# Optimization experiments

Hardware: AMD Instinct MI355X
Metric: run time of the kernel (lower is better)

The kernel has to match this reference:

```python
import jax, jax.numpy as jnp
import numpy as np

DIM = 256
H_GLOBAL = 8
H_LOCAL = 4  # max(1, num_heads // 2)
WINDOW = 5
HALF = WINDOW // 2
B, S = 4, 2048
EPS = 1e-5


def layer_norm(x, g, b):
    mu = jnp.mean(x, axis=-1, keepdims=True)
    var = jnp.mean(jnp.square(x - mu), axis=-1, keepdims=True)
    return (x - mu) * jax.lax.rsqrt(var + EPS) * g + b


def qkv_proj(x, in_w, in_b):
    qkv = x @ in_w.T + in_b
    return jnp.split(qkv, 3, axis=-1)


def global_mha(x, in_w, in_b, out_w, out_b, nh):
    Bq, Sq, D = x.shape
    hd = D // nh
    q, k, v = qkv_proj(x, in_w, in_b)
    q = q.reshape(Bq, Sq, nh, hd)
    k = k.reshape(Bq, Sq, nh, hd)
    v = v.reshape(Bq, Sq, nh, hd)
    scores = jnp.einsum('bqhd,bkhd->bhqk', q, k) / np.sqrt(hd).astype(np.float32)
    attn = jax.nn.softmax(scores, axis=-1)
    o = jnp.einsum('bhqk,bkhd->bqhd', attn, v).reshape(Bq, Sq, D)
    return o @ out_w.T + out_b


def local_mha(x, in_w, in_b, out_w, out_b, nh):
    # banded sliding-window attention, window = 2*HALF+1, per-query softmax
    Bq, Sq, D = x.shape
    hd = D // nh
    q, k, v = qkv_proj(x, in_w, in_b)
    kp = jnp.pad(k, ((0, 0), (HALF, HALF), (0, 0)))
    vp = jnp.pad(v, ((0, 0), (HALF, HALF), (0, 0)))
    # [B, S, W, D] windows of keys/values around each query position
    k_win = jnp.stack([kp[:, j:j + Sq] for j in range(WINDOW)], axis=2)
    v_win = jnp.stack([vp[:, j:j + Sq] for j in range(WINDOW)], axis=2)
    q = q.reshape(Bq, Sq, nh, hd)
    k_win = k_win.reshape(Bq, Sq, WINDOW, nh, hd)
    v_win = v_win.reshape(Bq, Sq, WINDOW, nh, hd)
    scores = jnp.einsum('bshd,bswhd->bshw', q, k_win) / np.sqrt(hd).astype(np.float32)
    idx = jnp.arange(Sq)[:, None] + jnp.arange(-HALF, HALF + 1)[None, :]  # [S, W]
    valid = (idx >= 0) & (idx < Sq)
    scores = jnp.where(valid[None, :, None, :], scores, -jnp.inf)
    attn = jax.nn.softmax(scores, axis=-1)
    o = jnp.einsum('bshw,bswhd->bshd', attn, v_win).reshape(Bq, Sq, D)
    return o @ out_w.T + out_b


def setup_inputs() -> dict:
    key = jax.random.key(0)
    ks = jax.random.split(key, 8)
    sc = 0.02
    d = DIM
    return {
        'x': jax.random.normal(ks[0], (B, S, d), jnp.float32),
        'g_in_w': jax.random.normal(ks[1], (3 * d, d), jnp.float32) * sc,
        'g_in_b': jnp.zeros((3 * d,), jnp.float32),
        'g_out_w': jax.random.normal(ks[2], (d, d), jnp.float32) * sc,
        'g_out_b': jnp.zeros((d,), jnp.float32),
        't_in_w': jax.random.normal(ks[3], (3 * d, d), jnp.float32) * sc,
        't_in_b': jnp.zeros((3 * d,), jnp.float32),
        't_out_w': jax.random.normal(ks[4], (d, d), jnp.float32) * sc,
        't_out_b': jnp.zeros((d,), jnp.float32),
        'fus_w1': jax.random.normal(ks[5], (2 * d, 2 * d), jnp.float32) * sc,
        'fus_b1': jnp.zeros((2 * d,), jnp.float32),
        'fus_w2': jax.random.normal(ks[6], (d, 2 * d), jnp.float32) * sc,
        'fus_b2': jnp.zeros((d,), jnp.float32),
        'ffn_w1': jax.random.normal(ks[7], (2 * d, d), jnp.float32) * sc,
        'ffn_b1': jnp.zeros((2 * d,), jnp.float32),
        'ffn_w2': jax.random.normal(jax.random.fold_in(key, 9), (d, 2 * d), jnp.float32) * sc,
        'ffn_b2': jnp.zeros((d,), jnp.float32),
        'gn_g': jnp.ones((d,), jnp.float32),
        'gn_b': jnp.zeros((d,), jnp.float32),
        'fn_g': jnp.ones((d,), jnp.float32),
        'fn_b': jnp.zeros((d,), jnp.float32),
    }


def reference(x, g_in_w, g_in_b, g_out_w, g_out_b,
              t_in_w, t_in_b, t_out_w, t_out_b,
              fus_w1, fus_b1, fus_w2, fus_b2,
              ffn_w1, ffn_b1, ffn_w2, ffn_b2,
              gn_g, gn_b, fn_g, fn_b):
    x_global = global_mha(x, g_in_w, g_in_b, g_out_w, g_out_b, H_GLOBAL)
    x_local = local_mha(x, t_in_w, t_in_b, t_out_w, t_out_b, H_LOCAL)
    x_comb = jnp.concatenate([x_global, x_local], axis=-1)
    x_fused = jax.nn.silu(x_comb @ fus_w1.T + fus_b1) @ fus_w2.T + fus_b2
    x = layer_norm(x + x_fused, gn_g, gn_b)
    x_ffn = jax.nn.silu(x @ ffn_w1.T + ffn_b1) @ ffn_w2.T + ffn_b2
    x = layer_norm(x + x_ffn, fn_g, fn_b)
    return x
```

## Files before the change

kernel.cpp:

```cpp
#include <hip/hip_runtime.h>

constexpr int Bb = 4;
constexpr int Ss = 2048;
constexpr int QSTR = 1536;

typedef __bf16 bf16x8 __attribute__((ext_vector_type(8)));
typedef __bf16 bf16x4 __attribute__((ext_vector_type(4)));
typedef float  f32x4  __attribute__((ext_vector_type(4)));
typedef unsigned int uint2v __attribute__((ext_vector_type(2)));
typedef unsigned int uint4v __attribute__((ext_vector_type(4)));

__device__ __forceinline__ void glds16(const void* g, void* l) {
    __builtin_amdgcn_global_load_lds(
        (const __attribute__((address_space(1))) unsigned int*)g,
        (__attribute__((address_space(3))) unsigned int*)l, 16, 0, 0);
}

__device__ __forceinline__ void xpose4(unsigned int& a, unsigned int& b) {
    uint2v r = __builtin_amdgcn_permlane32_swap(a, b, false, false);
    uint2v u = __builtin_amdgcn_permlane16_swap(r[0], r[1], false, false);
    a = u[0]; b = u[1];
}

__device__ __forceinline__ unsigned int exp2_pk(float a, float b) {
    float ea = __builtin_amdgcn_exp2f(a);
    float eb = __builtin_amdgcn_exp2f(b);
    unsigned int r;
    asm("v_cvt_pk_bf16_f32 %0, %1, %2" : "=v"(r) : "v"(ea), "v"(eb));
    return r;
}

struct CvtArgs {
    const float* src[9];
    __bf16* dst[9];
    int start[10];
};

__global__ __launch_bounds__(256) void convert_all(CvtArgs a)
{
    int e = 0;
    const int bid = blockIdx.x;
#pragma unroll
    for (int i = 0; i < 8; i++) if (bid >= a.start[i + 1]) e = i + 1;
    const int idx = (bid - a.start[e]) * 256 + threadIdx.x;
    const float* s = a.src[e];
    float4 v0 = *(const float4*)&s[(size_t)idx * 8];
    float4 v1 = *(const float4*)&s[(size_t)idx * 8 + 4];
    bf16x8 o;
    o[0] = (__bf16)v0.x; o[1] = (__bf16)v0.y; o[2] = (__bf16)v0.z; o[3] = (__bf16)v0.w;
    o[4] = (__bf16)v1.x; o[5] = (__bf16)v1.y; o[6] = (__bf16)v1.z; o[7] = (__bf16)v1.w;
    *(bf16x8*)&a.dst[e][(size_t)idx * 8] = o;
}

__global__ __launch_bounds__(256) void gemm128(
    const __bf16* __restrict__ A, const __bf16* __restrict__ W,
    const float* __restrict__ bias, const float* __restrict__ bias2, int bsplit,
    __bf16* __restrict__ C, int K, int ldc)
{
    __shared__ __bf16 As[128 * 64];
    __shared__ __bf16 Ws[128 * 64];
    const int tid = threadIdx.x;
    const int lane = tid & 63;
    const int wv = tid >> 6;
    const int wm = (wv >> 1) * 64;
    const int wn = (wv & 1) * 64;
    const int qrow = lane & 15;
    const int quad = lane >> 4;
    const int n0 = blockIdx.x * 128;
    const int m0 = blockIdx.y * 128;

    f32x4 acc[4][4];
#pragma unroll
    for (int i = 0; i < 4; i++)
#pragma unroll
        for (int j = 0; j < 4; j++) acc[i][j] = {0.f, 0.f, 0.f, 0.f};

    for (int k0 = 0; k0 < K; k0 += 64) {
        __syncthreads();
#pragma unroll
        for (int i = 0; i < 4; i++) {
            const int c = (wv * 4 + i) * 64 + lane;
            const int row = c >> 3, g = c & 7;
            const int gs = (g ^ (row & 7)) * 8;
            glds16(&A[(size_t)(m0 + row) * K + k0 + gs], &As[(wv * 4 + i) * 512]);
            glds16(&W[(size_t)(n0 + row) * K + k0 + gs], &Ws[(wv * 4 + i) * 512]);
        }
        __syncthreads();
#pragma unroll
        for (int ksub = 0; ksub < 2; ksub++) {
            const int gl = ksub * 4 + quad;
            bf16x8 af[4], bf[4];
#pragma unroll
            for (int mi = 0; mi < 4; mi++) {
                const int row = wm + mi * 16 + qrow;
                af[mi] = *(const bf16x8*)&As[row * 64 + (gl ^ (row & 7)) * 8];
            }
#pragma unroll
            for (int ni = 0; ni < 4; ni++) {
                const int row = wn + ni * 16 + qrow;
                bf[ni] = *(const bf16x8*)&Ws[row * 64 + (gl ^ (row & 7)) * 8];
            }
#pragma unroll
            for (int mi = 0; mi < 4; mi++)
#pragma unroll
                for (int ni = 0; ni < 4; ni++)
                    acc[mi][ni] = __builtin_amdgcn_mfma_f32_16x16x32_bf16(
                        af[mi], bf[ni], acc[mi][ni], 0, 0, 0);
        }
    }

    float bz[4];
#pragma unroll
    for (int ni = 0; ni < 4; ni++) {
        const int n = n0 + wn + ni * 16 + qrow;
        bz[ni] = (n < bsplit) ? bias[n] : bias2[n - bsplit];
    }
#pragma unroll
    for (int mi = 0; mi < 4; mi++)
#pragma unroll
        for (int r = 0; r < 4; r++) {
            const int row = m0 + wm + mi * 16 + quad * 4 + r;
#pragma unroll
            for (int ni = 0; ni < 4; ni++) {
                float v = acc[mi][ni][r] + bz[ni];
                C[(size_t)row * ldc + n0 + wn + ni * 16 + qrow] = (__bf16)v;
            }
        }
}

template<bool SILU, bool OUT_BF16>
__global__ __launch_bounds__(256) void gemm_mid(
    const __bf16* __restrict__ A0, const __bf16* __restrict__ W0,
    const float* __restrict__ bias0, const __bf16* __restrict__ W1,
    const float* __restrict__ bias1, int nsplit, int aoff1, int coff1,
    void* __restrict__ C, int lda, int K, int ldc)
{
    __shared__ __bf16 As[64 * 128];
    __shared__ __bf16 Ws[64 * 128];
    const int tid = threadIdx.x;
    const int lane = tid & 63;
    const int wv = tid >> 6;
    const int wm = (wv >> 1) * 32;
    const int wn = (wv & 1) * 32;
    const int qrow = lane & 15;
    const int quad = lane >> 4;
    const bool second = (int)blockIdx.x >= nsplit;
    const int bx = second ? (blockIdx.x - nsplit) : blockIdx.x;
    const __bf16* A = second ? (A0 + aoff1) : A0;
    const __bf16* W = second ? W1 : W0;
    const float* bias = second ? bias1 : bias0;
    const int coff = second ? coff1 : 0;
    const int n0 = bx * 64;
    const int m0 = blockIdx.y * 64;

    f32x4 acc[2][2];
#pragma unroll
    for (int i = 0; i < 2; i++)
#pragma unroll
        for (int j = 0; j < 2; j++) acc[i][j] = {0.f, 0.f, 0.f, 0.f};

    for (int k0 = 0; k0 < K; k0 += 128) {
        __syncthreads();
#pragma unroll
        for (int i = 0; i < 4; i++) {
            const int c = (wv * 4 + i) * 64 + lane;
            const int row = c >> 4, s = c & 15;
            const int gs = ((s & 8) | ((s ^ row) & 7)) * 8;
            glds16(&A[(size_t)(m0 + row) * lda + k0 + gs], &As[(wv * 4 + i) * 512]);
            glds16(&W[(size_t)(n0 + row) * K + k0 + gs], &Ws[(wv * 4 + i) * 512]);
        }
        __syncthreads();
#pragma unroll
        for (int ksub = 0; ksub < 4; ksub++) {
            const int gl = ksub * 4 + quad;
            bf16x8 af[2], bf[2];
#pragma unroll
            for (int mi = 0; mi < 2; mi++) {
                const int row = wm + mi * 16 + qrow;
                const int s = (gl & 8) | ((gl ^ row) & 7);
                af[mi] = *(const bf16x8*)&As[row * 128 + s * 8];
            }
#pragma unroll
            for (int ni = 0; ni < 2; ni++) {
                const int row = wn + ni * 16 + qrow;
                const int s = (gl & 8) | ((gl ^ row) & 7);
                bf[ni] = *(const bf16x8*)&Ws[row * 128 + s * 8];
            }
#pragma unroll
            for (int mi = 0; mi < 2; mi++)
#pragma unroll
                for (int ni = 0; ni < 2; ni++)
                    acc[mi][ni] = __builtin_amdgcn_mfma_f32_16x16x32_bf16(
                        af[mi], bf[ni], acc[mi][ni], 0, 0, 0);
        }
    }

    float bz[2];
#pragma unroll
    for (int ni = 0; ni < 2; ni++) bz[ni] = bias[n0 + wn + ni * 16 + qrow];

#pragma unroll
    for (int mi = 0; mi < 2; mi++)
#pragma unroll
        for (int r = 0; r < 4; r++) {
            const int row = m0 + wm + mi * 16 + quad * 4 + r;
#pragma unroll
            for (int ni = 0; ni < 2; ni++) {
                float v = acc[mi][ni][r] + bz[ni];
                if (SILU) v = v / (1.f + __expf(-v));
                const int col = coff + n0 + wn + ni * 16 + qrow;
                if (OUT_BF16)
                    ((__bf16*)C)[(size_t)row * ldc + col] = (__bf16)v;
                else
                    ((float*)C)[(size_t)row * ldc + col] = v;
            }
        }
}

__global__ __launch_bounds__(512) void attn_fused(
    const __bf16* __restrict__ qkv, __bf16* __restrict__ Op,
    float* __restrict__ Lp, __bf16* __restrict__ acat)
{
    __shared__ __bf16 Kl[2][64 * 32];
    __shared__ __bf16 Vt[2][32 * 72];

    const int t = threadIdx.x;
    const int lane = t & 63;
    const int wv = t >> 6;

    if (blockIdx.x < 1024) {
        const int bid = blockIdx.x;
        const int sp = bid & 3;
        const int qc = (bid >> 2) & 7;
        const int h  = (bid >> 5) & 7;
        const int b  = bid >> 8;
        const int bS = b * Ss;
        const int q0 = qc * 256;

        const int qrow = lane & 15;
        const int quad = lane >> 4;
        const float cQ = 1.4426950408889634f * 0.17677669529663687f;

        bf16x8 qf[2];
#pragma unroll
        for (int tl = 0; tl < 2; tl++) {
            bf16x8 qraw = *(const bf16x8*)(qkv +
                (size_t)(bS + q0 + wv * 32 + tl * 16 + qrow) * QSTR + h * 32 + quad * 8);
#pragma unroll
            for (int i = 0; i < 8; i++) qf[tl][i] = (__bf16)((float)qraw[i] * cQ);
        }
        bf16x8 ones;
#pragma unroll
        for (int i = 0; i < 8; i++) ones[i] = (__bf16)1.0f;

        f32x4 o0[2], o1[2], lac[2];
#pragma unroll
        for (int tl = 0; tl < 2; tl++) {
            o0[tl] = {0.f, 0.f, 0.f, 0.f};
            o1[tl] = {0.f, 0.f, 0.f, 0.f};
            lac[tl] = {0.f, 0.f, 0.f, 0.f};
        }
        const f32x4 z = {0.f, 0.f, 0.f, 0.f};

        const int kc_c = wv * 64 + lane;
        const int kkey = kc_c >> 2, kdg = kc_c & 3;
        const int vkey = t & 63, vq = t >> 6;
        const int kc0 = sp * 8;

        bf16x4 vreg = *(const bf16x4*)(qkv +
            (size_t)(bS + kc0 * 64 + vkey) * QSTR + 512 + h * 32 + vq * 4);
        if (wv < 4)
            glds16(qkv + (size_t)(bS + kc0 * 64 + kkey) * QSTR + 256 + h * 32 + kdg * 8,
                   &Kl[0][wv * 512]);

        for (int i = 0; i < 8; i++) {
            const int cur = i & 1;
#pragma unroll
            for (int e = 0; e < 4; e++) Vt[cur][(vq * 4 + e) * 72 + vkey] = vreg[e];
            __syncthreads();
            const int nx = (i < 7) ? (kc0 + i + 1) : (kc0 + 7);
            vreg = *(const bf16x4*)(qkv +
                (size_t)(bS + nx * 64 + vkey) * QSTR + 512 + h * 32 + vq * 4);
            if (i < 7 && wv < 4)
                glds16(qkv + (size_t)(bS + nx * 64 + kkey) * QSTR + 256 + h * 32 + kdg * 8,
                       &Kl[1 - cur][wv * 512]);

            bf16x8 kf[4];
#pragma unroll
            for (int kg = 0; kg < 4; kg++)
                kf[kg] = *(const bf16x8*)&Kl[cur][(kg * 16 + qrow) * 32 + quad * 8];
            bf16x8 vf00 = *(const bf16x8*)&Vt[cur][qrow * 72 + quad * 8];
            bf16x8 vf01 = *(const bf16x8*)&Vt[cur][qrow * 72 + 32 + quad * 8];
            bf16x8 vf10 = *(const bf16x8*)&Vt[cur][(16 + qrow) * 72 + quad * 8];
            bf16x8 vf11 = *(const bf16x8*)&Vt[cur][(16 + qrow) * 72 + 32 + quad * 8];

#pragma unroll
            for (int tl = 0; tl < 2; tl++) {
                f32x4 s[4];
#pragma unroll
                for (int kg = 0; kg < 4; kg++)
                    s[kg] = __builtin_amdgcn_mfma_f32_16x16x32_bf16(
                        kf[kg], qf[tl], z, 0, 0, 0);
                unsigned int R[4][2];
#pragma unroll
                for (int kg = 0; kg < 4; kg++) {
                    R[kg][0] = exp2_pk(s[kg][0], s[kg][1]);
                    R[kg][1] = exp2_pk(s[kg][2], s[kg][3]);
                }
                xpose4(R[0][0], R[1][0]);
                xpose4(R[0][1], R[1][1]);
                xpose4(R[2][0], R[3][0]);
                xpose4(R[2][1], R[3][1]);
                uint4v p0u = {R[0][0], R[0][1], R[1][0], R[1][1]};
                uint4v p1u = {R[2][0], R[2][1], R[3][0], R[3][1]};
                bf16x8 pf0 = __builtin_bit_cast(bf16x8, p0u);
                bf16x8 pf1 = __builtin_bit_cast(bf16x8, p1u);

                o0[tl] = __builtin_amdgcn_mfma_f32_16x16x32_bf16(vf00, pf0, o0[tl], 0, 0, 0);
                o1[tl] = __builtin_amdgcn_mfma_f32_16x16x32_bf16(vf10, pf0, o1[tl], 0, 0, 0);
                lac[tl] = __builtin_amdgcn_mfma_f32_16x16x32_bf16(ones, pf0, lac[tl], 0, 0, 0);
                o0[tl] = __builtin_amdgcn_mfma_f32_16x16x32_bf16(vf01, pf1, o0[tl], 0, 0, 0);
                o1[tl] = __builtin_amdgcn_mfma_f32_16x16x32_bf16(vf11, pf1, o1[tl], 0, 0, 0);
                lac[tl] = __builtin_amdgcn_mfma_f32_16x16x32_bf16(ones, pf1, lac[tl], 0, 0, 0);
            }
        }

#pragma unroll
        for (int tl = 0; tl < 2; tl++) {
            const int gid = (b * 8 + h) * 2048 + q0 + wv * 32 + tl * 16 + qrow;
            __bf16* po = Op + (size_t)sp * 2097152 + (size_t)gid * 32;
            bf16x4 w0, w1;
#pragma unroll
            for (int r = 0; r < 4; r++) {
                w0[r] = (__bf16)o0[tl][r];
                w1[r] = (__bf16)o1[tl][r];
            }
            *(bf16x4*)&po[quad * 4]      = w0;
            *(bf16x4*)&po[16 + quad * 4] = w1;
            if (quad == 0) Lp[sp * 65536 + gid] = lac[tl][0];
        }
    } else {
        const int w = (blockIdx.x - 1024) * 8 + wv;
        const int g = lane >> 3;
        const int l8 = lane & 7;
        const int R = w * 8 + g;
        const int h = R & 3;
        const int s = (R >> 2) & 2047;
        const int b = R >> 13;

        float qv[8];
        {
            bf16x8 q8 = *(const bf16x8*)&qkv[(size_t)(b * Ss + s) * QSTR + 768 + h * 64 + l8 * 8];
#pragma unroll
            for (int e = 0; e < 8; e++) qv[e] = (float)q8[e];
        }

        float sc[5];
        bf16x8 v8[5];
#pragma unroll
        for (int j = 0; j < 5; j++) {
            int pos = s + j - 2;
            bool valid = (pos >= 0) && (pos < Ss);
            int cpos = valid ? pos : 0;
            const size_t rb = (size_t)(b * Ss + cpos) * QSTR;
            bf16x8 k8 = *(const bf16x8*)&qkv[rb + 1024 + h * 64 + l8 * 8];
            v8[j]     = *(const bf16x8*)&qkv[rb + 1280 + h * 64 + l8 * 8];
            float p = 0.f;
#pragma unroll
            for (int e = 0; e < 8; e++) p += qv[e] * (float)k8[e];
            p += __shfl_xor(p, 1, 64);
            p += __shfl_xor(p, 2, 64);
            p += __shfl_xor(p, 4, 64);
            sc[j] = valid ? p * 0.125f : -1e30f;
        }
        float m = sc[0];
#pragma unroll
        for (int j = 1; j < 5; j++) m = fmaxf(m, sc[j]);
        float l = 0.f;
        float o[8];
#pragma unroll
        for (int e = 0; e < 8; e++) o[e] = 0.f;
#pragma unroll
        for (int j = 0; j < 5; j++) {
            float pe = __builtin_amdgcn_exp2f((sc[j] - m) * 1.4426950408889634f);
            l += pe;
#pragma unroll
            for (int e = 0; e < 8; e++) o[e] += pe * (float)v8[j][e];
        }
        const float li = 1.f / l;
        bf16x8 r;
#pragma unroll
        for (int e = 0; e < 8; e++) r[e] = (__bf16)(o[e] * li);
        *(bf16x8*)&acat[(size_t)(b * Ss + s) * 512 + 256 + h * 64 + l8 * 8] = r;
    }
}

__global__ __launch_bounds__(256) void attn_combine(
    const __bf16* __restrict__ Op, const float* __restrict__ Lp,
    __bf16* __restrict__ acat)
{
    const int t = blockIdx.x * 256 + threadIdx.x;
    const int gid = t >> 3;
    const int dg = t & 7;
    const int b = gid >> 14;
    const int h = (gid >> 11) & 7;
    const int q = gid & 2047;

    const float li = 1.f / (Lp[gid] + Lp[65536 + gid] +
                            Lp[131072 + gid] + Lp[196608 + gid]);
    const __bf16* base = Op + (size_t)gid * 32 + dg * 4;
    bf16x4 a0 = *(const bf16x4*)&base[0];
    bf16x4 a1 = *(const bf16x4*)&base[2097152];
    bf16x4 a2 = *(const bf16x4*)&base[4194304];
    bf16x4 a3 = *(const bf16x4*)&base[6291456];
    bf16x4 r;
#pragma unroll
    for (int i = 0; i < 4; i++)
        r[i] = (__bf16)(((float)a0[i] + (float)a1[i] +
                         (float)a2[i] + (float)a3[i]) * li);
    *(bf16x4*)&acat[(size_t)(b * Ss + q) * 512 + h * 32 + dg * 4] = r;
}

__global__ __launch_bounds__(256) void ln_residual(
    const float* __restrict__ a, const __bf16* __restrict__ r,
    const float* __restrict__ g, const float* __restrict__ be,
    float* __restrict__ out, __bf16* __restrict__ ob)
{
    const int lane = threadIdx.x & 63;
    const int tok = blockIdx.x * 4 + (threadIdx.x >> 6);
    float4 xa = ((const float4*)a)[(size_t)tok * 64 + lane];
    bf16x4 xr = *(const bf16x4*)&r[(size_t)tok * 256 + lane * 4];
    float4 x;
    x.x = xa.x + (float)xr[0]; x.y = xa.y + (float)xr[1];
    x.z = xa.z + (float)xr[2]; x.w = xa.w + (float)xr[3];
    float sum = x.x + x.y + x.z + x.w;
#pragma unroll
    for (int off = 32; off > 0; off >>= 1) sum += __shfl_xor(sum, off, 64);
    float mu = sum * (1.f / 256.f);
    float4 c;
    c.x = x.x - mu; c.y = x.y - mu; c.z = x.z - mu; c.w = x.w - mu;
    float sq = c.x * c.x + c.y * c.y + c.z * c.z + c.w * c.w;
#pragma unroll
    for (int off = 32; off > 0; off >>= 1) sq += __shfl_xor(sq, off, 64);
    float rs = rsqrtf(sq * (1.f / 256.f) + 1e-5f);
    float4 gg = ((const float4*)g)[lane];
    float4 bb = ((const float4*)be)[lane];
    float4 o;
    o.x = c.x * rs * gg.x + bb.x; o.y = c.y * rs * gg.y + bb.y;
    o.z = c.z * rs * gg.z + bb.z; o.w = c.w * rs * gg.w + bb.w;
    ((float4*)out)[(size_t)tok * 64 + lane] = o;
    if (ob) {
        bf16x4 hh;
        hh[0] = (__bf16)o.x; hh[1] = (__bf16)o.y; hh[2] = (__bf16)o.z; hh[3] = (__bf16)o.w;
        *(bf16x4*)&ob[(size_t)tok * 256 + lane * 4] = hh;
    }
}

extern "C" void kernel_launch(void* const* d_in, const int* in_sizes, int n_in,
                              void* d_out, int out_size, void* d_ws, size_t ws_size,
                              hipStream_t stream)
{
    const float* x      = (const float*)d_in[0];
    const float* g_in_w = (const float*)d_in[1];
    const float* g_in_b = (const float*)d_in[2];
    const float* g_out_w= (const float*)d_in[3];
    const float* g_out_b= (const float*)d_in[4];
    const float* t_in_w = (const float*)d_in[5];
    const float* t_in_b = (const float*)d_in[6];
    const float* t_out_w= (const float*)d_in[7];
    const float* t_out_b= (const float*)d_in[8];
    const float* fus_w1 = (const float*)d_in[9];
    const float* fus_b1 = (const float*)d_in[10];
    const float* fus_w2 = (const float*)d_in[11];
    const float* fus_b2 = (const float*)d_in[12];
    const float* ffn_w1 = (const float*)d_in[13];
    const float* ffn_b1 = (const float*)d_in[14];
    const float* ffn_w2 = (const float*)d_in[15];
    const float* ffn_b2 = (const float*)d_in[16];
    const float* gn_g   = (const float*)d_in[17];
    const float* gn_b   = (const float*)d_in[18];
    const float* fn_g   = (const float*)d_in[19];
    const float* fn_b   = (const float*)d_in[20];
    float* out = (float*)d_out;
    float* ws  = (float*)d_ws;

    __bf16* xb     = (__bf16*)(ws);
    __bf16* wb     = (__bf16*)(ws + 1048576);
    __bf16* qkvgl  = (__bf16*)(ws + 1638400);
    __bf16* acat   = (__bf16*)(ws + 7929856);
    __bf16* fcomb  = (__bf16*)(ws + 10027008);
    __bf16* h1     = (__bf16*)(ws + 12124160);
    __bf16* xfb    = (__bf16*)(ws + 14221312);
    float*  x2     = ws + 16318464;
    __bf16* x2b    = (__bf16*)(ws + 18415616);
    __bf16* h2     = h1;
    __bf16* xffb   = xfb;
    __bf16* Op = (__bf16*)(ws + 10027008);
    float*  Lp = ws + 18415616;

    __bf16* w_gin  = wb;
    __bf16* w_gout = wb + 393216;
    __bf16* w_tout = wb + 458752;
    __bf16* w_f1   = wb + 524288;
    __bf16* w_f2   = wb + 786432;
    __bf16* w_n1   = wb + 917504;
    __bf16* w_n2   = wb + 1048576;

    CvtArgs ca;
    ca.src[0] = x;      ca.dst[0] = xb;
    ca.src[1] = g_in_w; ca.dst[1] = w_gin;
    ca.src[2] = t_in_w; ca.dst[2] = w_gin + 196608;
    ca.src[3] = g_out_w;ca.dst[3] = w_gout;
    ca.src[4] = t_out_w;ca.dst[4] = w_tout;
    ca.src[5] = fus_w1; ca.dst[5] = w_f1;
    ca.src[6] = fus_w2; ca.dst[6] = w_f2;
    ca.src[7] = ffn_w1; ca.dst[7] = w_n1;
    ca.src[8] = ffn_w2; ca.dst[8] = w_n2;
    int st[10] = {0, 1024, 1120, 1216, 1248, 1280, 1408, 1472, 1536, 1600};
    for (int i = 0; i < 10; i++) ca.start[i] = st[i];

    convert_all<<<dim3(1600), 256, 0, stream>>>(ca);

    gemm128<<<dim3(12, 64), 256, 0, stream>>>(
        xb, w_gin, g_in_b, t_in_b, 768, qkvgl, 256, QSTR);
    attn_fused<<<dim3(1536), 512, 0, stream>>>(qkvgl, Op, Lp, acat);
    attn_combine<<<dim3(2048), 256, 0, stream>>>(Op, Lp, acat);
    gemm_mid<false, true><<<dim3(8, 128), 256, 0, stream>>>(
        acat, w_gout, g_out_b, w_tout, t_out_b, 4, 256, 256, fcomb, 512, 256, 512);
    gemm_mid<true,  true><<<dim3(8, 128), 256, 0, stream>>>(
        fcomb, w_f1, fus_b1, w_f1, fus_b1, 1 << 30, 0, 0, h1, 512, 512, 512);
    gemm_mid<false, true><<<dim3(4, 128), 256, 0, stream>>>(
        h1, w_f2, fus_b2, w_f2, fus_b2, 1 << 30, 0, 0, xfb, 512, 512, 256);
    ln_residual<<<dim3(2048), 256, 0, stream>>>(x, xfb, gn_g, gn_b, x2, x2b);
    gemm_mid<true,  true><<<dim3(8, 128), 256, 0, stream>>>(
        x2b, w_n1, ffn_b1, w_n1, ffn_b1, 1 << 30, 0, 0, h2, 256, 256, 512);
    gemm_mid<false, true><<<dim3(4, 128), 256, 0, stream>>>(
        h2, w_n2, ffn_b2, w_n2, ffn_b2, 1 << 30, 0, 0, xffb, 512, 512, 256);
    ln_residual<<<dim3(2048), 256, 0, stream>>>(x2, xffb, fn_g, fn_b, out, nullptr);
}
```

Measured before the change: 210.7 us.

## Fuse attention combine, projections, MLPs and layernorms into one per-token epilogue kernel

Replaces the attention-combine kernel, six mid-size GEMM launches and two layernorm kernels with a single epilogue kernel. Each 64-thread wavefront handles 16 tokens and keeps all intermediate activations in registers, chaining MFMA stages through a transpose-pack helper. Weights are read straight from global memory without LDS staging. This removes many launches and the intermediate HBM round-trips, but it brings heavy register pressure, only 512 single-wave blocks (low occupancy), and repeated uncoalesced weight reads from cache.

```diff
diff --git a/kernel.cpp b/kernel.cpp
--- a/kernel.cpp
+++ b/kernel.cpp
@@ -22,12 +22,88 @@
     a = u[0]; b = u[1];
 }
 
+__device__ __forceinline__ unsigned int cvtpk(float a, float b) {
+    unsigned int r;
+    asm("v_cvt_pk_bf16_f32 %0, %1, %2" : "=v"(r) : "v"(a), "v"(b));
+    return r;
+}
+
 __device__ __forceinline__ unsigned int exp2_pk(float a, float b) {
     float ea = __builtin_amdgcn_exp2f(a);
     float eb = __builtin_amdgcn_exp2f(b);
-    unsigned int r;
-    asm("v_cvt_pk_bf16_f32 %0, %1, %2" : "=v"(r) : "v"(ea), "v"(eb));
-    return r;
+    return cvtpk(ea, eb);
+}
+
+__device__ __forceinline__ bf16x8 pack_pair(f32x4 dA, f32x4 dB) {
+    unsigned int RA0 = cvtpk(dA[0], dA[1]);
+    unsigned int RA1 = cvtpk(dA[2], dA[3]);
+    unsigned int RB0 = cvtpk(dB[0], dB[1]);
+    unsigned int RB1 = cvtpk(dB[2], dB[3]);
+    xpose4(RA0, RB0);
+    xpose4(RA1, RB1);
+    uint4v u = {RA0, RA1, RB0, RB1};
+    return __builtin_bit_cast(bf16x8, u);
+}
+
+template<int NK>
+__device__ __forceinline__ void mm4(
+    const __bf16* __restrict__ W, const int K, const int ft0,
+    const bf16x8* act, const int qrow, const int quad, f32x4 acc[4])
+{
+#pragma unroll
+    for (int i = 0; i < 4; i++) acc[i] = {0.f, 0.f, 0.f, 0.f};
+#pragma unroll
+    for (int kc = 0; kc < NK; kc++) {
+        bf16x8 wf[4];
+#pragma unroll
+        for (int i = 0; i < 4; i++)
+            wf[i] = *(const bf16x8*)&W[(size_t)((ft0 + i) * 16 + qrow) * K + kc * 32 + quad * 8];
+#pragma unroll
+        for (int i = 0; i < 4; i++)
+            acc[i] = __builtin_amdgcn_mfma_f32_16x16x32_bf16(wf[i], act[kc], acc[i], 0, 0, 0);
+    }
+}
+
+template<int NK, bool SILU>
+__device__ __forceinline__ void stage_pack4(
+    const __bf16* __restrict__ W, const int K, const int ft0,
+    const float* __restrict__ bias,
+    const bf16x8* act, const int qrow, const int quad, bf16x8* outc)
+{
+    f32x4 acc[4];
+    mm4<NK>(W, K, ft0, act, qrow, quad, acc);
+#pragma unroll
+    for (int i = 0; i < 4; i++) {
+        float4 bz = *(const float4*)&bias[(ft0 + i) * 16 + quad * 4];
+        acc[i][0] += bz.x; acc[i][1] += bz.y; acc[i][2] += bz.z; acc[i][3] += bz.w;
+        if (SILU) {
+#pragma unroll
+            for (int r = 0; r < 4; r++) {
+                float v = acc[i][r];
+                acc[i][r] = v / (1.f + __builtin_amdgcn_exp2f(-v * 1.4426950408889634f));
+            }
+        }
+    }
+    outc[0] = pack_pair(acc[0], acc[1]);
+    outc[1] = pack_pair(acc[2], acc[3]);
+}
+
+template<int NK>
+__device__ __forceinline__ void stage_d4(
+    const __bf16* __restrict__ W, const int K, const int ft0,
+    const float* __restrict__ bias,
+    const bf16x8* act, const int qrow, const int quad, f32x4* dout)
+{
+    f32x4 acc[4];
+    mm4<NK>(W, K, ft0, act, qrow, quad, acc);
+#pragma unroll
+    for (int i = 0; i < 4; i++) {
+        float4 bz = *(const float4*)&bias[(ft0 + i) * 16 + quad * 4];
+        dout[i][0] = acc[i][0] + bz.x;
+        dout[i][1] = acc[i][1] + bz.y;
+        dout[i][2] = acc[i][2] + bz.z;
+        dout[i][3] = acc[i][3] + bz.w;
+    }
 }
 
 struct CvtArgs {
@@ -124,95 +200,6 @@
             for (int ni = 0; ni < 4; ni++) {
                 float v = acc[mi][ni][r] + bz[ni];
                 C[(size_t)row * ldc + n0 + wn + ni * 16 + qrow] = (__bf16)v;
-            }
-        }
-}
-
-template<bool SILU, bool OUT_BF16>
-__global__ __launch_bounds__(256) void gemm_mid(
-    const __bf16* __restrict__ A0, const __bf16* __restrict__ W0,
-    const float* __restrict__ bias0, const __bf16* __restrict__ W1,
-    const float* __restrict__ bias1, int nsplit, int aoff1, int coff1,
-    void* __restrict__ C, int lda, int K, int ldc)
-{
-    __shared__ __bf16 As[64 * 128];
-    __shared__ __bf16 Ws[64 * 128];
-    const int tid = threadIdx.x;
-    const int lane = tid & 63;
-    const int wv = tid >> 6;
-    const int wm = (wv >> 1) * 32;
-    const int wn = (wv & 1) * 32;
-    const int qrow = lane & 15;
-    const int quad = lane >> 4;
-    const bool second = (int)blockIdx.x >= nsplit;
-    const int bx = second ? (blockIdx.x - nsplit) : blockIdx.x;
-    const __bf16* A = second ? (A0 + aoff1) : A0;
-    const __bf16* W = second ? W1 : W0;
-    const float* bias = second ? bias1 : bias0;
-    const int coff = second ? coff1 : 0;
-    const int n0 = bx * 64;
-    const int m0 = blockIdx.y * 64;
-
-    f32x4 acc[2][2];
-#pragma unroll
-    for (int i = 0; i < 2; i++)
-#pragma unroll
-        for (int j = 0; j < 2; j++) acc[i][j] = {0.f, 0.f, 0.f, 0.f};
-
-    for (int k0 = 0; k0 < K; k0 += 128) {
-        __syncthreads();
-#pragma unroll
-        for (int i = 0; i < 4; i++) {
-            const int c = (wv * 4 + i) * 64 + lane;
-            const int row = c >> 4, s = c & 15;
-            const int gs = ((s & 8) | ((s ^ row) & 7)) * 8;
-            glds16(&A[(size_t)(m0 + row) * lda + k0 + gs], &As[(wv * 4 + i) * 512]);
-            glds16(&W[(size_t)(n0 + row) * K + k0 + gs], &Ws[(wv * 4 + i) * 512]);
-        }
-        __syncthreads();
-#pragma unroll
-        for (int ksub = 0; ksub < 4; ksub++) {
-            const int gl = ksub * 4 + quad;
-            bf16x8 af[2], bf[2];
-#pragma unroll
-            for (int mi = 0; mi < 2; mi++) {
-                const int row = wm + mi * 16 + qrow;
-                const int s = (gl & 8) | ((gl ^ row) & 7);
-                af[mi] = *(const bf16x8*)&As[row * 128 + s * 8];
-            }
-#pragma unroll
-            for (int ni = 0; ni < 2; ni++) {
-                const int row = wn + ni * 16 + qrow;
-                const int s = (gl & 8) | ((gl ^ row) & 7);
-                bf[ni] = *(const bf16x8*)&Ws[row * 128 + s * 8];
-            }
-#pragma unroll
-            for (int mi = 0; mi < 2; mi++)
-#pragma unroll
-                for (int ni = 0; ni < 2; ni++)
-                    acc[mi][ni] = __builtin_amdgcn_mfma_f32_16x16x32_bf16(
-                        af[mi], bf[ni], acc[mi][ni], 0, 0, 0);
-        }
-    }
-
-    float bz[2];
-#pragma unroll
-    for (int ni = 0; ni < 2; ni++) bz[ni] = bias[n0 + wn + ni * 16 + qrow];
-
-#pragma unroll
-    for (int mi = 0; mi < 2; mi++)
-#pragma unroll
-        for (int r = 0; r < 4; r++) {
-            const int row = m0 + wm + mi * 16 + quad * 4 + r;
-#pragma unroll
-            for (int ni = 0; ni < 2; ni++) {
-                float v = acc[mi][ni][r] + bz[ni];
-                if (SILU) v = v / (1.f + __expf(-v));
-                const int col = coff + n0 + wn + ni * 16 + qrow;
-                if (OUT_BF16)
-                    ((__bf16*)C)[(size_t)row * ldc + col] = (__bf16)v;
-                else
-                    ((float*)C)[(size_t)row * ldc + col] = v;
             }
         }
 }
@@ -395,64 +382,142 @@
     }
 }
 
-__global__ __launch_bounds__(256) void attn_combine(
+__global__ __launch_bounds__(64) void epilogue(
     const __bf16* __restrict__ Op, const float* __restrict__ Lp,
-    __bf16* __restrict__ acat)
-{
-    const int t = blockIdx.x * 256 + threadIdx.x;
-    const int gid = t >> 3;
-    const int dg = t & 7;
-    const int b = gid >> 14;
-    const int h = (gid >> 11) & 7;
-    const int q = gid & 2047;
-
-    const float li = 1.f / (Lp[gid] + Lp[65536 + gid] +
-                            Lp[131072 + gid] + Lp[196608 + gid]);
-    const __bf16* base = Op + (size_t)gid * 32 + dg * 4;
-    bf16x4 a0 = *(const bf16x4*)&base[0];
-    bf16x4 a1 = *(const bf16x4*)&base[2097152];
-    bf16x4 a2 = *(const bf16x4*)&base[4194304];
-    bf16x4 a3 = *(const bf16x4*)&base[6291456];
-    bf16x4 r;
-#pragma unroll
-    for (int i = 0; i < 4; i++)
-        r[i] = (__bf16)(((float)a0[i] + (float)a1[i] +
-                         (float)a2[i] + (float)a3[i]) * li);
-    *(bf16x4*)&acat[(size_t)(b * Ss + q) * 512 + h * 32 + dg * 4] = r;
-}
-
-__global__ __launch_bounds__(256) void ln_residual(
-    const float* __restrict__ a, const __bf16* __restrict__ r,
-    const float* __restrict__ g, const float* __restrict__ be,
-    float* __restrict__ out, __bf16* __restrict__ ob)
+    const __bf16* __restrict__ acat, const float* __restrict__ x,
+    const __bf16* __restrict__ w_gout, const float* __restrict__ g_out_b,
+    const __bf16* __restrict__ w_tout, const float* __restrict__ t_out_b,
+    const __bf16* __restrict__ w_f1, const float* __restrict__ fus_b1,
+    const __bf16* __restrict__ w_f2, const float* __restrict__ fus_b2,
+    const __bf16* __restrict__ w_n1, const float* __restrict__ ffn_b1,
+    const __bf16* __restrict__ w_n2, const float* __restrict__ ffn_b2,
+    const float* __restrict__ gn_g, const float* __restrict__ gn_b,
+    const float* __restrict__ fn_g, const float* __restrict__ fn_b,
+    float* __restrict__ out)
 {
     const int lane = threadIdx.x & 63;
-    const int tok = blockIdx.x * 4 + (threadIdx.x >> 6);
-    float4 xa = ((const float4*)a)[(size_t)tok * 64 + lane];
-    bf16x4 xr = *(const bf16x4*)&r[(size_t)tok * 256 + lane * 4];
-    float4 x;
-    x.x = xa.x + (float)xr[0]; x.y = xa.y + (float)xr[1];
-    x.z = xa.z + (float)xr[2]; x.w = xa.w + (float)xr[3];
-    float sum = x.x + x.y + x.z + x.w;
-#pragma unroll
-    for (int off = 32; off > 0; off >>= 1) sum += __shfl_xor(sum, off, 64);
-    float mu = sum * (1.f / 256.f);
-    float4 c;
-    c.x = x.x - mu; c.y = x.y - mu; c.z = x.z - mu; c.w = x.w - mu;
-    float sq = c.x * c.x + c.y * c.y + c.z * c.z + c.w * c.w;
-#pragma unroll
-    for (int off = 32; off > 0; off >>= 1) sq += __shfl_xor(sq, off, 64);
-    float rs = rsqrtf(sq * (1.f / 256.f) + 1e-5f);
-    float4 gg = ((const float4*)g)[lane];
-    float4 bb = ((const float4*)be)[lane];
-    float4 o;
-    o.x = c.x * rs * gg.x + bb.x; o.y = c.y * rs * gg.y + bb.y;
-    o.z = c.z * rs * gg.z + bb.z; o.w = c.w * rs * gg.w + bb.w;
-    ((float4*)out)[(size_t)tok * 64 + lane] = o;
-    if (ob) {
-        bf16x4 hh;
-        hh[0] = (__bf16)o.x; hh[1] = (__bf16)o.y; hh[2] = (__bf16)o.z; hh[3] = (__bf16)o.w;
-        *(bf16x4*)&ob[(size_t)tok * 256 + lane * 4] = hh;
+    const int qrow = lane & 15;
+    const int quad = lane >> 4;
+    const int t = blockIdx.x * 16 + qrow;
+    const int b = t >> 11;
+    const int q = t & 2047;
+
+    bf16x8 act0[16];
+#pragma unroll
+    for (int h = 0; h < 8; h++) {
+        const size_t gid = (size_t)(b * 8 + h) * 2048 + q;
+        const float li = 1.f / (Lp[gid] + Lp[65536 + gid] +
+                                Lp[131072 + gid] + Lp[196608 + gid]);
+        const __bf16* base = Op + gid * 32 + quad * 8;
+        bf16x8 a0 = *(const bf16x8*)&base[0];
+        bf16x8 a1 = *(const bf16x8*)&base[2097152];
+        bf16x8 a2 = *(const bf16x8*)&base[4194304];
+        bf16x8 a3 = *(const bf16x8*)&base[6291456];
+        unsigned int w[4];
+#pragma unroll
+        for (int p = 0; p < 4; p++) {
+            float v0 = ((float)a0[2*p]   + (float)a1[2*p]   +
+                        (float)a2[2*p]   + (float)a3[2*p])   * li;
+            float v1 = ((float)a0[2*p+1] + (float)a1[2*p+1] +
+                        (float)a2[2*p+1] + (float)a3[2*p+1]) * li;
+            w[p] = cvtpk(v0, v1);
+        }
+        uint4v u = {w[0], w[1], w[2], w[3]};
+        act0[h] = __builtin_bit_cast(bf16x8, u);
+    }
+#pragma unroll
+    for (int c = 0; c < 8; c++)
+        act0[8 + c] = *(const bf16x8*)&acat[(size_t)t * 512 + 256 + c * 32 + quad * 8];
+
+    bf16x8 act1[16];
+#pragma unroll
+    for (int g4 = 0; g4 < 4; g4++)
+        stage_pack4<8, false>(w_gout, 256, g4 * 4, g_out_b, act0, qrow, quad, &act1[g4 * 2]);
+#pragma unroll
+    for (int g4 = 0; g4 < 4; g4++)
+        stage_pack4<8, false>(w_tout, 256, g4 * 4, t_out_b, act0 + 8, qrow, quad, &act1[8 + g4 * 2]);
+
+    bf16x8 act2[16];
+#pragma unroll
+    for (int g4 = 0; g4 < 8; g4++)
+        stage_pack4<16, true>(w_f1, 512, g4 * 4, fus_b1, act1, qrow, quad, &act2[g4 * 2]);
+
+    f32x4 d[16];
+#pragma unroll
+    for (int g4 = 0; g4 < 4; g4++)
+        stage_d4<16>(w_f2, 512, g4 * 4, fus_b2, act2, qrow, quad, &d[g4 * 4]);
+
+#pragma unroll
+    for (int ft = 0; ft < 16; ft++) {
+        float4 xr = *(const float4*)&x[(size_t)t * 256 + ft * 16 + quad * 4];
+        d[ft][0] += xr.x; d[ft][1] += xr.y; d[ft][2] += xr.z; d[ft][3] += xr.w;
+    }
+    float s = 0.f;
+#pragma unroll
+    for (int ft = 0; ft < 16; ft++) s += d[ft][0] + d[ft][1] + d[ft][2] + d[ft][3];
+    s += __shfl_xor(s, 16, 64);
+    s += __shfl_xor(s, 32, 64);
+    const float mu = s * (1.f / 256.f);
+    float sq = 0.f;
+#pragma unroll
+    for (int ft = 0; ft < 16; ft++)
+#pragma unroll
+        for (int r = 0; r < 4; r++) { d[ft][r] -= mu; sq += d[ft][r] * d[ft][r]; }
+    sq += __shfl_xor(sq, 16, 64);
+    sq += __shfl_xor(sq, 32, 64);
+    const float rs = rsqrtf(sq * (1.f / 256.f) + 1e-5f);
+#pragma unroll
+    for (int ft = 0; ft < 16; ft++) {
+        float4 gg = *(const float4*)&gn_g[ft * 16 + quad * 4];
+        float4 bb = *(const float4*)&gn_b[ft * 16 + quad * 4];
+        d[ft][0] = d[ft][0] * rs * gg.x + bb.x;
+        d[ft][1] = d[ft][1] * rs * gg.y + bb.y;
+        d[ft][2] = d[ft][2] * rs * gg.z + bb.z;
+        d[ft][3] = d[ft][3] * rs * gg.w + bb.w;
+    }
+    bf16x8 actx2[8];
+#pragma unroll
+    for (int c = 0; c < 8; c++)
+        actx2[c] = pack_pair(d[2 * c], d[2 * c + 1]);
+
+    bf16x8 act5[16];
+#pragma unroll
+    for (int g4 = 0; g4 < 8; g4++)
+        stage_pack4<8, true>(w_n1, 256, g4 * 4, ffn_b1, actx2, qrow, quad, &act5[g4 * 2]);
+
+    f32x4 d5[16];
+#pragma unroll
+    for (int g4 = 0; g4 < 4; g4++)
+        stage_d4<16>(w_n2, 512, g4 * 4, ffn_b2, act5, qrow, quad, &d5[g4 * 4]);
+#pragma unroll
+    for (int ft = 0; ft < 16; ft++)
+#pragma unroll
+        for (int r = 0; r < 4; r++) d5[ft][r] += d[ft][r];
+
+    float s2 = 0.f;
+#pragma unroll
+    for (int ft = 0; ft < 16; ft++) s2 += d5[ft][0] + d5[ft][1] + d5[ft][2] + d5[ft][3];
+    s2 += __shfl_xor(s2, 16, 64);
+    s2 += __shfl_xor(s2, 32, 64);
+    const float mu2 = s2 * (1.f / 256.f);
+    float sq2 = 0.f;
+#pragma unroll
+    for (int ft = 0; ft < 16; ft++)
+#pragma unroll
+        for (int r = 0; r < 4; r++) { d5[ft][r] -= mu2; sq2 += d5[ft][r] * d5[ft][r]; }
+    sq2 += __shfl_xor(sq2, 16, 64);
+    sq2 += __shfl_xor(sq2, 32, 64);
+    const float rs2 = rsqrtf(sq2 * (1.f / 256.f) + 1e-5f);
+#pragma unroll
+    for (int ft = 0; ft < 16; ft++) {
+        float4 gg = *(const float4*)&fn_g[ft * 16 + quad * 4];
+        float4 bb = *(const float4*)&fn_b[ft * 16 + quad * 4];
+        f32x4 o;
+        o[0] = d5[ft][0] * rs2 * gg.x + bb.x;
+        o[1] = d5[ft][1] * rs2 * gg.y + bb.y;
+        o[2] = d5[ft][2] * rs2 * gg.z + bb.z;
+        o[3] = d5[ft][3] * rs2 * gg.w + bb.w;
+        *(f32x4*)&out[(size_t)t * 256 + ft * 16 + quad * 4] = o;
     }
 }
 
@@ -488,13 +553,6 @@
     __bf16* wb     = (__bf16*)(ws + 1048576);
     __bf16* qkvgl  = (__bf16*)(ws + 1638400);
     __bf16* acat   = (__bf16*)(ws + 7929856);
-    __bf16* fcomb  = (__bf16*)(ws + 10027008);
-    __bf16* h1     = (__bf16*)(ws + 12124160);
-    __bf16* xfb    = (__bf16*)(ws + 14221312);
-    float*  x2     = ws + 16318464;
-    __bf16* x2b    = (__bf16*)(ws + 18415616);
-    __bf16* h2     = h1;
-    __bf16* xffb   = xfb;
     __bf16* Op = (__bf16*)(ws + 10027008);
     float*  Lp = ws + 18415616;
 
@@ -524,17 +582,10 @@
     gemm128<<<dim3(12, 64), 256, 0, stream>>>(
         xb, w_gin, g_in_b, t_in_b, 768, qkvgl, 256, QSTR);
     attn_fused<<<dim3(1536), 512, 0, stream>>>(qkvgl, Op, Lp, acat);
-    attn_combine<<<dim3(2048), 256, 0, stream>>>(Op, Lp, acat);
-    gemm_mid<false, true><<<dim3(8, 128), 256, 0, stream>>>(
-        acat, w_gout, g_out_b, w_tout, t_out_b, 4, 256, 256, fcomb, 512, 256, 512);
-    gemm_mid<true,  true><<<dim3(8, 128), 256, 0, stream>>>(
-        fcomb, w_f1, fus_b1, w_f1, fus_b1, 1 << 30, 0, 0, h1, 512, 512, 512);
-    gemm_mid<false, true><<<dim3(4, 128), 256, 0, stream>>>(
-        h1, w_f2, fus_b2, w_f2, fus_b2, 1 << 30, 0, 0, xfb, 512, 512, 256);
-    ln_residual<<<dim3(2048), 256, 0, stream>>>(x, xfb, gn_g, gn_b, x2, x2b);
-    gemm_mid<true,  true><<<dim3(8, 128), 256, 0, stream>>>(
-        x2b, w_n1, ffn_b1, w_n1, ffn_b1, 1 << 30, 0, 0, h2, 256, 256, 512);
-    gemm_mid<false, true><<<dim3(4, 128), 256, 0, stream>>>(
-        h2, w_n2, ffn_b2, w_n2, ffn_b2, 1 << 30, 0, 0, xffb, 512, 512, 256);
-    ln_residual<<<dim3(2048), 256, 0, stream>>>(x2, xffb, fn_g, fn_b, out, nullptr);
-}
+    epilogue<<<dim3(512), 64, 0, stream>>>(
+        Op, Lp, acat, x,
+        w_gout, g_out_b, w_tout, t_out_b,
+        w_f1, fus_b1, w_f2, fus_b2,
+        w_n1, ffn_b1, w_n2, ffn_b2,
+        gn_g, gn_b, fn_g, fn_b, out);
+}
```

New measurement: 260.2 us. 1.23x slower.

## Fuse second FFN/fusion GEMMs with residual add and LayerNorm

Applied to the files above, without the earlier changes.

Adds a gemm_ln kernel in which each block computes a full 16-row by 256-column output tile, then adds bias and residual and applies LayerNorm in-register using shuffles and a small shared reduction. It replaces the pairs of gemm_mid (N=256) plus ln_residual launches, removing two launches and the bf16 intermediate round-trip. The trade-off is that each block stages the whole 256x128 weight slice in LDS for only 16 rows, so weight traffic per row rises and blocks are LDS-heavy, which lowers occupancy. The residual is now read in fp32 straight from global memory with a strided access pattern.

```diff
diff --git a/kernel.cpp b/kernel.cpp
--- a/kernel.cpp
+++ b/kernel.cpp
@@ -217,6 +217,130 @@
         }
 }
 
+template<bool OBF>
+__global__ __launch_bounds__(256) void gemm_ln(
+    const __bf16* __restrict__ A, const __bf16* __restrict__ W,
+    const float* __restrict__ bias, const float* __restrict__ res,
+    const float* __restrict__ g, const float* __restrict__ be,
+    float* __restrict__ out, __bf16* __restrict__ outb)
+{
+    __shared__ __bf16 As[16 * 128];
+    __shared__ __bf16 Ws[256 * 128];
+    __shared__ float lnp[2][16][4];
+    const int tid = threadIdx.x;
+    const int lane = tid & 63;
+    const int wv = tid >> 6;
+    const int qrow = lane & 15;
+    const int quad = lane >> 4;
+    const int m0 = blockIdx.x * 16;
+
+    f32x4 acc[4];
+#pragma unroll
+    for (int ni = 0; ni < 4; ni++) acc[ni] = {0.f, 0.f, 0.f, 0.f};
+
+    for (int k0 = 0; k0 < 512; k0 += 128) {
+        __syncthreads();
+        {
+            const int c = wv * 64 + lane;
+            const int row = c >> 4, s = c & 15;
+            const int gs = ((s & 8) | ((s ^ row) & 7)) * 8;
+            glds16(&A[(size_t)(m0 + row) * 512 + k0 + gs], &As[wv * 512]);
+        }
+#pragma unroll
+        for (int i = 0; i < 16; i++) {
+            const int c = (wv * 16 + i) * 64 + lane;
+            const int row = c >> 4, s = c & 15;
+            const int gs = ((s & 8) | ((s ^ row) & 7)) * 8;
+            glds16(&W[(size_t)row * 512 + k0 + gs], &Ws[(wv * 16 + i) * 512]);
+        }
+        __syncthreads();
+#pragma unroll
+        for (int ksub = 0; ksub < 4; ksub++) {
+            const int gl = ksub * 4 + quad;
+            bf16x8 af, bf[4];
+            {
+                const int row = qrow;
+                const int s = (gl & 8) | ((gl ^ row) & 7);
+                af = *(const bf16x8*)&As[row * 128 + s * 8];
+            }
+#pragma unroll
+            for (int ni = 0; ni < 4; ni++) {
+                const int row = wv * 64 + ni * 16 + qrow;
+                const int s = (gl & 8) | ((gl ^ row) & 7);
+                bf[ni] = *(const bf16x8*)&Ws[row * 128 + s * 8];
+            }
+#pragma unroll
+            for (int ni = 0; ni < 4; ni++)
+                acc[ni] = __builtin_amdgcn_mfma_f32_16x16x32_bf16(
+                    af, bf[ni], acc[ni], 0, 0, 0);
+        }
+    }
+
+    f32x4 d[4];
+#pragma unroll
+    for (int ni = 0; ni < 4; ni++) {
+        const int f = wv * 64 + ni * 16 + qrow;
+        const float bz = bias[f];
+#pragma unroll
+        for (int r = 0; r < 4; r++)
+            d[ni][r] = acc[ni][r] + bz + res[(size_t)(m0 + quad * 4 + r) * 256 + f];
+    }
+
+    f32x4 ps;
+#pragma unroll
+    for (int r = 0; r < 4; r++) ps[r] = d[0][r] + d[1][r] + d[2][r] + d[3][r];
+#pragma unroll
+    for (int off = 1; off <= 8; off <<= 1)
+#pragma unroll
+        for (int r = 0; r < 4; r++) ps[r] += __shfl_xor(ps[r], off, 64);
+    if (qrow == 0)
+#pragma unroll
+        for (int r = 0; r < 4; r++) lnp[0][quad * 4 + r][wv] = ps[r];
+    __syncthreads();
+    float mu[4];
+#pragma unroll
+    for (int r = 0; r < 4; r++) {
+        const int t = quad * 4 + r;
+        mu[r] = (lnp[0][t][0] + lnp[0][t][1] + lnp[0][t][2] + lnp[0][t][3]) * (1.f / 256.f);
+    }
+
+#pragma unroll
+    for (int r = 0; r < 4; r++) {
+        float a0 = d[0][r] - mu[r], a1 = d[1][r] - mu[r];
+        float a2 = d[2][r] - mu[r], a3 = d[3][r] - mu[r];
+        ps[r] = a0 * a0 + a1 * a1 + a2 * a2 + a3 * a3;
+    }
+#pragma unroll
+    for (int off = 1; off <= 8; off <<= 1)
+#pragma unroll
+        for (int r = 0; r < 4; r++) ps[r] += __shfl_xor(ps[r], off, 64);
+    if (qrow == 0)
+#pragma unroll
+        for (int r = 0; r < 4; r++) lnp[1][quad * 4 + r][wv] = ps[r];
+    __syncthreads();
+    float rsv[4];
+#pragma unroll
+    for (int r = 0; r < 4; r++) {
+        const int t = quad * 4 + r;
+        float v = (lnp[1][t][0] + lnp[1][t][1] + lnp[1][t][2] + lnp[1][t][3]) * (1.f / 256.f);
+        rsv[r] = rsqrtf(v + 1e-5f);
+    }
+
+#pragma unroll
+    for (int ni = 0; ni < 4; ni++) {
+        const int f = wv * 64 + ni * 16 + qrow;
+        const float gg = g[f];
+        const float bb = be[f];
+#pragma unroll
+        for (int r = 0; r < 4; r++) {
+            const size_t idx = (size_t)(m0 + quad * 4 + r) * 256 + f;
+            float o = (d[ni][r] - mu[r]) * rsv[r] * gg + bb;
+            out[idx] = o;
+            if (OBF) outb[idx] = (__bf16)o;
+        }
+    }
+}
+
 __global__ __launch_bounds__(512) void attn_fused(
     const __bf16* __restrict__ qkv, __bf16* __restrict__ Op,
     float* __restrict__ Lp, __bf16* __restrict__ acat)
@@ -419,41 +543,6 @@
         r[i] = (__bf16)(((float)a0[i] + (float)a1[i] +
                          (float)a2[i] + (float)a3[i]) * li);
     *(bf16x4*)&acat[(size_t)(b * Ss + q) * 512 + h * 32 + dg * 4] = r;
-}
-
-__global__ __launch_bounds__(256) void ln_residual(
-    const float* __restrict__ a, const __bf16* __restrict__ r,
-    const float* __restrict__ g, const float* __restrict__ be,
-    float* __restrict__ out, __bf16* __restrict__ ob)
-{
-    const int lane = threadIdx.x & 63;
-    const int tok = blockIdx.x * 4 + (threadIdx.x >> 6);
-    float4 xa = ((const float4*)a)[(size_t)tok * 64 + lane];
-    bf16x4 xr = *(const bf16x4*)&r[(size_t)tok * 256 + lane * 4];
-    float4 x;
-    x.x = xa.x + (float)xr[0]; x.y = xa.y + (float)xr[1];
-    x.z = xa.z + (float)xr[2]; x.w = xa.w + (float)xr[3];
-    float sum = x.x + x.y + x.z + x.w;
-#pragma unroll
-    for (int off = 32; off > 0; off >>= 1) sum += __shfl_xor(sum, off, 64);
-    float mu = sum * (1.f / 256.f);
-    float4 c;
-    c.x = x.x - mu; c.y = x.y - mu; c.z = x.z - mu; c.w = x.w - mu;
-    float sq = c.x * c.x + c.y * c.y + c.z * c.z + c.w * c.w;
-#pragma unroll
-    for (int off = 32; off > 0; off >>= 1) sq += __shfl_xor(sq, off, 64);
-    float rs = rsqrtf(sq * (1.f / 256.f) + 1e-5f);
-    float4 gg = ((const float4*)g)[lane];
-    float4 bb = ((const float4*)be)[lane];
-    float4 o;
-    o.x = c.x * rs * gg.x + bb.x; o.y = c.y * rs * gg.y + bb.y;
-    o.z = c.z * rs * gg.z + bb.z; o.w = c.w * rs * gg.w + bb.w;
-    ((float4*)out)[(size_t)tok * 64 + lane] = o;
-    if (ob) {
-        bf16x4 hh;
-        hh[0] = (__bf16)o.x; hh[1] = (__bf16)o.y; hh[2] = (__bf16)o.z; hh[3] = (__bf16)o.w;
-        *(bf16x4*)&ob[(size_t)tok * 256 + lane * 4] = hh;
-    }
 }
 
 extern "C" void kernel_launch(void* const* d_in, const int* in_sizes, int n_in,
@@ -490,11 +579,9 @@
     __bf16* acat   = (__bf16*)(ws + 7929856);
     __bf16* fcomb  = (__bf16*)(ws + 10027008);
     __bf16* h1     = (__bf16*)(ws + 12124160);
-    __bf16* xfb    = (__bf16*)(ws + 14221312);
     float*  x2     = ws + 16318464;
     __bf16* x2b    = (__bf16*)(ws + 18415616);
     __bf16* h2     = h1;
-    __bf16* xffb   = xfb;
     __bf16* Op = (__bf16*)(ws + 10027008);
     float*  Lp = ws + 18415616;
 
@@ -529,12 +616,10 @@
         acat, w_gout, g_out_b, w_tout, t_out_b, 4, 256, 256, fcomb, 512, 256, 512);
     gemm_mid<true,  true><<<dim3(8, 128), 256, 0, stream>>>(
         fcomb, w_f1, fus_b1, w_f1, fus_b1, 1 << 30, 0, 0, h1, 512, 512, 512);
-    gemm_mid<false, true><<<dim3(4, 128), 256, 0, stream>>>(
-        h1, w_f2, fus_b2, w_f2, fus_b2, 1 << 30, 0, 0, xfb, 512, 512, 256);
-    ln_residual<<<dim3(2048), 256, 0, stream>>>(x, xfb, gn_g, gn_b, x2, x2b);
+    gemm_ln<true><<<dim3(512), 256, 0, stream>>>(
+        h1, w_f2, fus_b2, x, gn_g, gn_b, x2, x2b);
     gemm_mid<true,  true><<<dim3(8, 128), 256, 0, stream>>>(
         x2b, w_n1, ffn_b1, w_n1, ffn_b1, 1 << 30, 0, 0, h2, 256, 256, 512);
-    gemm_mid<false, true><<<dim3(4, 128), 256, 0, stream>>>(
-        h2, w_n2, ffn_b2, w_n2, ffn_b2, 1 << 30, 0, 0, xffb, 512, 512, 256);
-    ln_residual<<<dim3(2048), 256, 0, stream>>>(x2, xffb, fn_g, fn_b, out, nullptr);
-}
+    gemm_ln<false><<<dim3(512), 256, 0, stream>>>(
+        h2, w_n2, ffn_b2, x2, fn_g, fn_b, out, nullptr);
+}
```

Result: no change. 207.2 us (-1.7%).
